# Optimization experiments

Hardware: AMD Instinct MI355X
Metric: run time of the kernel (lower is better)

Reference implementation:

```python
import jax, jax.numpy as jnp
import numpy as np

L = 2048      # max_length / encoder sequence length
E = 1024      # eo_hidden_size
H = 1024      # hidden_size
D = 512       # embed_size
V = 32000     # vocab_size
MV = 32768    # max_vocab_size


def setup_inputs() -> dict:
    key = jax.random.key(0)
    ks = jax.random.split(key, 20)
    s = 0.02
    return {
        "inp": jax.random.randint(ks[0], (1,), 0, V),
        "hidden": jax.random.normal(ks[1], (1, 1, H), jnp.float32),
        "encoder_outputs": jax.random.normal(ks[2], (L, E), jnp.float32),
        "input_seq": jax.random.randint(ks[3], (L,), 0, MV),
        "pre_prob": jax.random.randint(ks[4], (L,), 0, 2),
        "emb": jax.random.normal(ks[5], (V, D), jnp.float32) * s,
        "attn_W": jax.random.normal(ks[6], (L, H + D), jnp.float32) * s,
        "attn_b": jnp.zeros((L,), jnp.float32),
        "comb_W": jax.random.normal(ks[7], (H, E + D), jnp.float32) * s,
        "comb_b": jnp.zeros((H,), jnp.float32),
        "W_ih": jax.random.normal(ks[8], (3 * H, H + E), jnp.float32) * s,
        "W_hh": jax.random.normal(ks[9], (3 * H, H), jnp.float32) * s,
        "b_ih": jnp.zeros((3 * H,), jnp.float32),
        "b_hh": jnp.zeros((3 * H,), jnp.float32),
        "Wo_W": jax.random.normal(ks[10], (V, H), jnp.float32) * s,
        "Wo_b": jnp.zeros((V,), jnp.float32),
        "Wc_W": jax.random.normal(ks[11], (H, E), jnp.float32) * s,
        "Wc_b": jnp.zeros((H,), jnp.float32),
    }


def reference(inp, hidden, encoder_outputs, input_seq, pre_prob,
              emb, attn_W, attn_b, comb_W, comb_b,
              W_ih, W_hh, b_ih, b_hh, Wo_W, Wo_b, Wc_W, Wc_b):
    tok = inp[0]
    # --- copy-mechanism selective read (int path, matches torch .long() trunc) ---
    sel_w = (input_seq == tok).astype(jnp.int32) * pre_prob.astype(jnp.int32)  # [L]
    eo_int = jax.lax.stop_gradient(encoder_outputs).astype(jnp.int32)          # trunc toward 0
    sel_reading = (sel_w @ eo_int).astype(jnp.float32)                          # [E]
    # --- embedding (OOV -> UNK id 2); dropout is identity in eval ---
    embed_idx = jnp.where(tok >= V, 2, tok)
    embedded = emb[embed_idx]                                                   # [D]
    h = hidden[0, 0]                                                            # [H]
    # --- attention over encoder outputs ---
    attn_weights = jax.nn.softmax(attn_W @ jnp.concatenate([embedded, h]) + attn_b)  # [L]
    attn_applied = attn_weights @ encoder_outputs                               # [E]
    out = jax.nn.relu(comb_W @ jnp.concatenate([embedded, attn_applied]) + comb_b)   # [H]
    # --- single GRU step (torch gate order: r, z, n) ---
    x = jnp.concatenate([out, sel_reading])                                     # [H+E]
    gi = W_ih @ x + b_ih
    gh = W_hh @ h + b_hh
    r = jax.nn.sigmoid(gi[:H] + gh[:H])
    z = jax.nn.sigmoid(gi[H:2 * H] + gh[H:2 * H])
    n = jnp.tanh(gi[2 * H:] + r * gh[2 * H:])
    h_new = (1.0 - z) * n + z * h                                               # [H]
    # --- generate vs copy scores ---
    score_g = Wo_W @ h_new + Wo_b                                               # [V]
    score_c = jnp.tanh(encoder_outputs @ Wc_W.T + Wc_b) @ h_new                 # [L]
    score = jax.nn.softmax(jnp.concatenate([score_g, score_c]))                 # [V+L]
    prob_g, prob_c = score[:V], score[V:]
    # pad generate probs to MV and scatter-add copy probs (== mm with one-hot)
    out1 = jnp.zeros((MV,), score.dtype).at[:V].set(prob_g)
    out1 = out1.at[input_seq].add(prob_c)
    out1 = jnp.where(out1 == 0, 1e-9, out1)
    out1 = out1.at[2].set(1e-9)
    out1 = jnp.log(out1)
    return (out1[None, :], h_new[None, None, :], attn_weights[None, :], prob_c[None, :])
```

## Files before the change

### kernel.cpp

```cpp
#include <hip/hip_runtime.h>
#include <math.h>

#define LQ 2048
#define EQ 1024
#define HQ 1024
#define DQ 512
#define VQ 32000
#define MVQ 32768

#define OUT1_OFF 0
#define HNEW_OFF 32768
#define AW_OFF   33792
#define PC_OFF   35840

#define PSZ 2097152
#define KSPLIT 4

typedef __attribute__((ext_vector_type(8))) short short8_t;
typedef __attribute__((ext_vector_type(8))) unsigned short ushort8_t;
typedef __attribute__((ext_vector_type(4))) float floatx4;

__device__ inline float wred(float v) {
    v += __shfl_down(v, 32);
    v += __shfl_down(v, 16);
    v += __shfl_down(v, 8);
    v += __shfl_down(v, 4);
    v += __shfl_down(v, 2);
    v += __shfl_down(v, 1);
    return v;
}
__device__ inline float wred_max(float v) {
    v = fmaxf(v, __shfl_down(v, 32));
    v = fmaxf(v, __shfl_down(v, 16));
    v = fmaxf(v, __shfl_down(v, 8));
    v = fmaxf(v, __shfl_down(v, 4));
    v = fmaxf(v, __shfl_down(v, 2));
    v = fmaxf(v, __shfl_down(v, 1));
    return v;
}
__device__ inline float sigmoidf_(float x) { return 1.0f / (1.0f + expf(-x)); }
__device__ inline unsigned short f2bf(float x) {
    unsigned int u = __float_as_uint(x);
    unsigned int r = (u + 0x7fffu + ((u >> 16) & 1u)) >> 16;
    return (unsigned short)r;
}
__device__ inline float bf2f(unsigned short b) {
    return __uint_as_float(((unsigned int)b) << 16);
}
__device__ __forceinline__ void gload16(const unsigned short* g,
                                        unsigned short* l) {
    __builtin_amdgcn_global_load_lds(
        (const __attribute__((address_space(1))) unsigned int*)g,
        (__attribute__((address_space(3))) unsigned int*)l, 16, 0, 0);
}

__global__ __launch_bounds__(256) void k_prep(
    const float* __restrict__ enc, const float* __restrict__ Wc,
    const int* __restrict__ inp, const int* __restrict__ input_seq,
    const int* __restrict__ pre_prob,
    const float* __restrict__ attn_W, const float* __restrict__ attn_b,
    const float* __restrict__ emb, const float* __restrict__ hidden,
    unsigned short* __restrict__ Ah, unsigned short* __restrict__ Al,
    unsigned short* __restrict__ Bh, unsigned short* __restrict__ Bl,
    float* __restrict__ x2, float* __restrict__ logits, float* __restrict__ aa)
{
    __shared__ int s_cnt;
    __shared__ int s_list[LQ];
    const int tid = threadIdx.x;
    const int bx = blockIdx.x;
    if (bx < 512) {
        if (bx < 4) aa[bx * 256 + tid] = 0.0f;
        int warp = tid >> 6, lane = tid & 63;
        int r = bx * 4 + warp;
        int tok = inp[0];
        int ei = (tok >= VQ) ? 2 : tok;
        const float4* Wr = (const float4*)(attn_W + (size_t)r * 1536);
        const float4* e4 = (const float4*)(emb + (size_t)ei * DQ);
        const float4* h4 = (const float4*)hidden;
        float acc = 0.0f;
        #pragma unroll
        for (int i = 0; i < 6; ++i) {
            int idx = lane + i * 64;
            float4 x = (idx < 128) ? e4[idx] : h4[idx - 128];
            float4 w = Wr[idx];
            acc += w.x * x.x + w.y * x.y + w.z * x.z + w.w * x.w;
        }
        acc = wred(acc);
        if (lane == 0) logits[r] = acc + attn_b[r];
        return;
    }
    if (bx == 512) {
        if (tid == 0) s_cnt = 0;
        __syncthreads();
        int tok = inp[0];
        for (int l = tid; l < LQ; l += 256) {
            if (input_seq[l] == tok && pre_prob[l] != 0) {
                int p = atomicAdd(&s_cnt, 1);
                s_list[p] = l;
            }
        }
        __syncthreads();
        int nm = s_cnt;
        for (int e = tid; e < EQ; e += 256) {
            int acc = 0;
            for (int j = 0; j < nm; ++j)
                acc += (int)enc[(size_t)s_list[j] * EQ + e];
            x2[HQ + e] = (float)acc;
        }
        return;
    }
    size_t e0 = ((size_t)(bx - 513) * 256 + tid) * 8;
    const float* src;
    unsigned short *hdst, *ldst;
    size_t off;
    if (e0 < (size_t)LQ * EQ) { src = enc; hdst = Ah; ldst = Al; off = e0; }
    else { src = Wc; hdst = Bh; ldst = Bl; off = e0 - (size_t)LQ * EQ; }
    float4 v0 = *(const float4*)(src + off);
    float4 v1 = *(const float4*)(src + off + 4);
    float vv[8] = {v0.x, v0.y, v0.z, v0.w, v1.x, v1.y, v1.z, v1.w};
    ushort8_t H, L;
    #pragma unroll
    for (int k = 0; k < 8; ++k) {
        float x = vv[k];
        unsigned short hb = f2bf(x);
        H[k] = hb;
        L[k] = f2bf(x - bf2f(hb));
    }
    *(ushort8_t*)(hdst + off) = H;
    *(ushort8_t*)(ldst + off) = L;
}

__global__ __launch_bounds__(256, 2) void k_gemm_mfma(
    const unsigned short* __restrict__ Ah, const unsigned short* __restrict__ Al,
    const unsigned short* __restrict__ Bh, const unsigned short* __restrict__ Bl,
    float* __restrict__ P)
{
    __shared__ unsigned short sm[4 * 8192];
    const int t = threadIdx.x;
    const int lane = t & 63, wid = t >> 6;
    const int n0 = blockIdx.x * 128;
    const int m0 = blockIdx.y * 128;
    const int kz = blockIdx.z * 256;
    float* Pz = P + (size_t)blockIdx.z * PSZ;

    const unsigned short* tsrc =
        (wid == 0) ? Ah + (size_t)m0 * EQ :
        (wid == 1) ? Al + (size_t)m0 * EQ :
        (wid == 2) ? Bh + (size_t)n0 * EQ :
                     Bl + (size_t)n0 * EQ;
    unsigned short* tdst = sm + wid * 8192;

    const int srow = lane >> 3;
    const int schunk = lane & 7;
    const int wm = (wid >> 1) * 64, wn = (wid & 1) * 64;
    const int fr = lane & 15, kg = lane >> 4;

    floatx4 acc[4][4];
    #pragma unroll
    for (int i = 0; i < 4; ++i)
        #pragma unroll
        for (int j = 0; j < 4; ++j)
            acc[i][j] = (floatx4){0.f, 0.f, 0.f, 0.f};

    for (int s = 0; s < 4; ++s) {
        #pragma unroll
        for (int c = 0; c < 16; ++c) {
            int row = c * 8 + srow;
            int gch = schunk ^ (row & 7);
            gload16(tsrc + (size_t)row * EQ + kz + s * 64 + gch * 8,
                    tdst + c * 512);
        }
        __syncthreads();
        #pragma unroll
        for (int kk = 0; kk < 2; ++kk) {
            short8_t fah[4], fal[4], fbh[4], fbl[4];
            #pragma unroll
            for (int f = 0; f < 4; ++f) {
                int rowa = wm + f * 16 + fr;
                int ba = rowa * 128 + ((kk * 4 + kg) ^ (rowa & 7)) * 16;
                fah[f] = *(const short8_t*)((const char*)sm + ba);
                fal[f] = *(const short8_t*)((const char*)sm + 16384 + ba);
                int rowb = wn + f * 16 + fr;
                int bb = rowb * 128 + ((kk * 4 + kg) ^ (rowb & 7)) * 16;
                fbh[f] = *(const short8_t*)((const char*)sm + 32768 + bb);
                fbl[f] = *(const short8_t*)((const char*)sm + 49152 + bb);
            }
            #pragma unroll
            for (int i = 0; i < 4; ++i)
                #pragma unroll
                for (int j = 0; j < 4; ++j) {
                    acc[i][j] = __builtin_amdgcn_mfma_f32_16x16x32_bf16(
                        fah[i], fbh[j], acc[i][j], 0, 0, 0);
                    acc[i][j] = __builtin_amdgcn_mfma_f32_16x16x32_bf16(
                        fal[i], fbh[j], acc[i][j], 0, 0, 0);
                    acc[i][j] = __builtin_amdgcn_mfma_f32_16x16x32_bf16(
                        fah[i], fbl[j], acc[i][j], 0, 0, 0);
                }
        }
        __syncthreads();
    }
    #pragma unroll
    for (int i = 0; i < 4; ++i)
        #pragma unroll
        for (int j = 0; j < 4; ++j) {
            int row = m0 + wm + i * 16 + kg * 4;
            int col = n0 + wn + j * 16 + fr;
            #pragma unroll
            for (int r = 0; r < 4; ++r)
                Pz[(size_t)(row + r) * HQ + col] = acc[i][j][r];
        }
}

__global__ __launch_bounds__(256) void k_attn_sm_apply(
    const float* __restrict__ logits, const float* __restrict__ enc,
    float* __restrict__ aa, float* __restrict__ aw_out)
{
    __shared__ float sred[4];
    __shared__ float s_w[128];
    int tid = threadIdx.x, wid = tid >> 6, lane = tid & 63;
    float m = -3.4e38f;
    for (int i = tid; i < LQ; i += 256) m = fmaxf(m, logits[i]);
    m = wred_max(m);
    if (lane == 0) sred[wid] = m;
    __syncthreads();
    if (tid == 0)
        sred[0] = fmaxf(fmaxf(sred[0], sred[1]), fmaxf(sred[2], sred[3]));
    __syncthreads();
    m = sred[0];
    __syncthreads();
    float s = 0.0f;
    for (int i = tid; i < LQ; i += 256) s += expf(logits[i] - m);
    s = wred(s);
    if (lane == 0) sred[wid] = s;
    __syncthreads();
    if (tid == 0) sred[0] = sred[0] + sred[1] + sred[2] + sred[3];
    __syncthreads();
    s = sred[0];
    int l0 = blockIdx.y * 128;
    if (tid < 128) {
        float w = expf(logits[l0 + tid] - m) / s;
        s_w[tid] = w;
        if (blockIdx.x == 0) aw_out[l0 + tid] = w;
    }
    __syncthreads();
    int e = blockIdx.x * 256 + tid;
    float acc = 0.0f;
    for (int l = 0; l < 128; ++l)
        acc = fmaf(s_w[l], enc[(size_t)(l0 + l) * EQ + e], acc);
    atomicAdd(&aa[e], acc);
}

__global__ __launch_bounds__(256) void k_comb(
    const float* __restrict__ W, const float* __restrict__ b,
    const int* __restrict__ inp, const float* __restrict__ emb,
    const float* __restrict__ aa, float* __restrict__ x2)
{
    int warp = threadIdx.x >> 6, lane = threadIdx.x & 63;
    int r = blockIdx.x * 4 + warp;
    int tok = inp[0];
    int ei = (tok >= VQ) ? 2 : tok;
    const float4* Wr = (const float4*)(W + (size_t)r * 1536);
    const float4* e4 = (const float4*)(emb + (size_t)ei * DQ);
    const float4* a4 = (const float4*)aa;
    float acc = 0.0f;
    #pragma unroll
    for (int i = 0; i < 6; ++i) {
        int idx = lane + i * 64;
        float4 x = (idx < 128) ? e4[idx] : a4[idx - 128];
        float4 w = Wr[idx];
        acc += w.x * x.x + w.y * x.y + w.z * x.z + w.w * x.w;
    }
    acc = wred(acc);
    if (lane == 0) x2[r] = fmaxf(acc + b[r], 0.0f);
}

__global__ __launch_bounds__(256) void k_gru(
    const float* __restrict__ W_ih, const float* __restrict__ W_hh,
    const float* __restrict__ b_ih, const float* __restrict__ b_hh,
    const float* __restrict__ x2, const float* __restrict__ h,
    float* __restrict__ hnew, float* __restrict__ out_h)
{
    int warp = threadIdx.x >> 6, lane = threadIdx.x & 63;
    int i = blockIdx.x * 4 + warp;
    const float4* xv = (const float4*)x2;
    const float4* hv = (const float4*)h;
    const float4* Wr = (const float4*)(W_ih + (size_t)i * 2048);
    const float4* Wz = (const float4*)(W_ih + (size_t)(HQ + i) * 2048);
    const float4* Wn = (const float4*)(W_ih + (size_t)(2 * HQ + i) * 2048);
    const float4* Ur = (const float4*)(W_hh + (size_t)i * 1024);
    const float4* Uz = (const float4*)(W_hh + (size_t)(HQ + i) * 1024);
    const float4* Un = (const float4*)(W_hh + (size_t)(2 * HQ + i) * 1024);
    float ar = 0, az = 0, an = 0, br = 0, bz = 0, bn = 0;
    #pragma unroll
    for (int c = 0; c < 8; ++c) {
        int idx = lane + c * 64;
        float4 x = xv[idx];
        float4 w = Wr[idx]; ar += w.x*x.x + w.y*x.y + w.z*x.z + w.w*x.w;
        w = Wz[idx];        az += w.x*x.x + w.y*x.y + w.z*x.z + w.w*x.w;
        w = Wn[idx];        an += w.x*x.x + w.y*x.y + w.z*x.z + w.w*x.w;
    }
    #pragma unroll
    for (int c = 0; c < 4; ++c) {
        int idx = lane + c * 64;
        float4 x = hv[idx];
        float4 w = Ur[idx]; br += w.x*x.x + w.y*x.y + w.z*x.z + w.w*x.w;
        w = Uz[idx];        bz += w.x*x.x + w.y*x.y + w.z*x.z + w.w*x.w;
        w = Un[idx];        bn += w.x*x.x + w.y*x.y + w.z*x.z + w.w*x.w;
    }
    ar = wred(ar); az = wred(az); an = wred(an);
    br = wred(br); bz = wred(bz); bn = wred(bn);
    if (lane == 0) {
        float r = sigmoidf_(ar + b_ih[i] + br + b_hh[i]);
        float z = sigmoidf_(az + b_ih[HQ + i] + bz + b_hh[HQ + i]);
        float n = tanhf(an + b_ih[2 * HQ + i] + r * (bn + b_hh[2 * HQ + i]));
        float hn = (1.0f - z) * n + z * h[i];
        hnew[i] = hn;
        out_h[i] = hn;
    }
}

__global__ __launch_bounds__(256) void k_scores(
    const float* __restrict__ Wo_W, const float* __restrict__ Wo_b,
    const float* __restrict__ P, const float* __restrict__ Wc_b,
    const float* __restrict__ hnew, float* __restrict__ score)
{
    int warp = threadIdx.x >> 6, lane = threadIdx.x & 63;
    int r = blockIdx.x * 4 + warp;
    const float4* hv = (const float4*)hnew;
    float acc = 0.0f;
    if (r < VQ) {
        const float4* Wr = (const float4*)(Wo_W + (size_t)r * HQ);
        #pragma unroll
        for (int i = 0; i < 4; ++i) {
            int idx = lane + i * 64;
            float4 w = Wr[idx], x = hv[idx];
            acc += w.x * x.x + w.y * x.y + w.z * x.z + w.w * x.w;
        }
        acc = wred(acc);
        if (lane == 0) score[r] = acc + Wo_b[r];
    } else {
        int l = r - VQ;
        const float4* P0 = (const float4*)(P + (size_t)l * HQ);
        const float4* P1 = (const float4*)(P + (size_t)PSZ + (size_t)l * HQ);
        const float4* P2 = (const float4*)(P + 2 * (size_t)PSZ + (size_t)l * HQ);
        const float4* P3 = (const float4*)(P + 3 * (size_t)PSZ + (size_t)l * HQ);
        #pragma unroll
        for (int i = 0; i < 4; ++i) {
            int idx = lane + i * 64;
            float4 a = P0[idx], b1 = P1[idx], b2 = P2[idx], b3 = P3[idx];
            float4 bb = *(const float4*)(Wc_b + idx * 4);
            float4 x = hv[idx];
            acc += tanhf(a.x + b1.x + b2.x + b3.x + bb.x) * x.x +
                   tanhf(a.y + b1.y + b2.y + b3.y + bb.y) * x.y +
                   tanhf(a.z + b1.z + b2.z + b3.z + bb.z) * x.z +
                   tanhf(a.w + b1.w + b2.w + b3.w + bb.w) * x.w;
        }
        acc = wred(acc);
        if (lane == 0) score[VQ + l] = acc;
    }
}

__global__ __launch_bounds__(256) void k_final(
    const float* __restrict__ score, const int* __restrict__ input_seq,
    float* __restrict__ out1, float* __restrict__ out_pc)
{
    __shared__ float sred[4];
    __shared__ float bins[256];
    const int N = VQ + LQ;
    int tid = threadIdx.x, wid = tid >> 6, lane = tid & 63;
    float m = -3.4e38f;
    for (int i = tid; i < N; i += 256) m = fmaxf(m, score[i]);
    m = wred_max(m);
    if (lane == 0) sred[wid] = m;
    __syncthreads();
    if (tid == 0)
        sred[0] = fmaxf(fmaxf(sred[0], sred[1]), fmaxf(sred[2], sred[3]));
    __syncthreads();
    m = sred[0];
    __syncthreads();
    float s = 0.0f;
    for (int i = tid; i < N; i += 256) s += expf(score[i] - m);
    s = wred(s);
    if (lane == 0) sred[wid] = s;
    __syncthreads();
    if (tid == 0) sred[0] = sred[0] + sred[1] + sred[2] + sred[3];
    __syncthreads();
    s = sred[0];
    bins[tid] = 0.0f;
    __syncthreads();
    int i0 = blockIdx.x * 256;
    for (int l = tid; l < LQ; l += 256) {
        int si = input_seq[l];
        if (si >= i0 && si < i0 + 256)
            atomicAdd(&bins[si - i0], expf(score[VQ + l] - m) / s);
    }
    if (blockIdx.x < 8) {
        int l = blockIdx.x * 256 + tid;
        out_pc[l] = expf(score[VQ + l] - m) / s;
    }
    __syncthreads();
    int i = i0 + tid;
    float v = ((i < VQ) ? expf(score[i] - m) / s : 0.0f) + bins[tid];
    if (i == 2 || v == 0.0f) v = 1e-9f;
    out1[i] = logf(v);
}

extern "C" void kernel_launch(void* const* d_in, const int* in_sizes, int n_in,
                              void* d_out, int out_size, void* d_ws, size_t ws_size,
                              hipStream_t stream) {
    const int*   inp       = (const int*)  d_in[0];
    const float* hidden    = (const float*)d_in[1];
    const float* enc       = (const float*)d_in[2];
    const int*   input_seq = (const int*)  d_in[3];
    const int*   pre_prob  = (const int*)  d_in[4];
    const float* emb       = (const float*)d_in[5];
    const float* attn_W    = (const float*)d_in[6];
    const float* attn_b    = (const float*)d_in[7];
    const float* comb_W    = (const float*)d_in[8];
    const float* comb_b    = (const float*)d_in[9];
    const float* W_ih      = (const float*)d_in[10];
    const float* W_hh      = (const float*)d_in[11];
    const float* b_ih      = (const float*)d_in[12];
    const float* b_hh      = (const float*)d_in[13];
    const float* Wo_W      = (const float*)d_in[14];
    const float* Wo_b      = (const float*)d_in[15];
    const float* Wc_W      = (const float*)d_in[16];
    const float* Wc_b      = (const float*)d_in[17];

    float* out = (float*)d_out;

    unsigned short* Ah = (unsigned short*)d_ws;
    unsigned short* Al = Ah + (size_t)LQ * EQ;
    unsigned short* Bh = Al + (size_t)LQ * EQ;
    unsigned short* Bl = Bh + (size_t)HQ * EQ;
    float* P      = (float*)(Bl + (size_t)HQ * EQ);
    float* x2     = P + (size_t)KSPLIT * PSZ;
    float* hnew   = x2 + 2048;
    float* logits = hnew + 1024;
    float* aa     = logits + 2048;
    float* score  = aa + 1024;

    k_prep<<<2049, 256, 0, stream>>>(enc, Wc_W, inp, input_seq, pre_prob,
                                     attn_W, attn_b, emb, hidden,
                                     Ah, Al, Bh, Bl, x2, logits, aa);
    k_gemm_mfma<<<dim3(HQ / 128, LQ / 128, KSPLIT), 256, 0, stream>>>(
        Ah, Al, Bh, Bl, P);
    k_attn_sm_apply<<<dim3(EQ / 256, 16), 256, 0, stream>>>(logits, enc, aa,
                                                            out + AW_OFF);
    k_comb<<<HQ / 4, 256, 0, stream>>>(comb_W, comb_b, inp, emb, aa, x2);
    k_gru<<<HQ / 4, 256, 0, stream>>>(W_ih, W_hh, b_ih, b_hh, x2, hidden,
                                      hnew, out + HNEW_OFF);
    k_scores<<<(VQ + LQ) / 4, 256, 0, stream>>>(Wo_W, Wo_b, P, Wc_b, hnew,
                                                score);
    k_final<<<MVQ / 256, 256, 0, stream>>>(score, input_seq, out + OUT1_OFF,
                                           out + PC_OFF);
}
```

Measured before the change: 124.0 us.

## Fuse post-GEMM decoder stages into one cooperative kernel with grid syncs

Replaces the five small launches (attention softmax/apply, combine, GRU, scores, final softmax/scatter) and the non-conversion parts of the prep kernel with a single cooperative kernel of 512 blocks that uses grid-wide syncs between stages. The aim is to remove per-launch overhead and tail gaps between dependent small kernels. In exchange, the scores stage now loops over rows with fewer blocks, grid.sync costs replace launch boundaries, and the attention logits and selective read no longer overlap with the bf16 split conversion but run after the GEMM.

Result: slower. 395.4 us (+219.0%).

```diff
diff --git a/kernel.cpp b/kernel.cpp
--- a/kernel.cpp
+++ b/kernel.cpp
@@ -1,5 +1,8 @@
 #include <hip/hip_runtime.h>
+#include <hip/hip_cooperative_groups.h>
 #include <math.h>
+
+namespace cg = cooperative_groups;
 
 #define LQ 2048
 #define EQ 1024
@@ -54,62 +57,12 @@
         (__attribute__((address_space(3))) unsigned int*)l, 16, 0, 0);
 }
 
-__global__ __launch_bounds__(256) void k_prep(
+__global__ __launch_bounds__(256) void k_prep_split(
     const float* __restrict__ enc, const float* __restrict__ Wc,
-    const int* __restrict__ inp, const int* __restrict__ input_seq,
-    const int* __restrict__ pre_prob,
-    const float* __restrict__ attn_W, const float* __restrict__ attn_b,
-    const float* __restrict__ emb, const float* __restrict__ hidden,
     unsigned short* __restrict__ Ah, unsigned short* __restrict__ Al,
-    unsigned short* __restrict__ Bh, unsigned short* __restrict__ Bl,
-    float* __restrict__ x2, float* __restrict__ logits, float* __restrict__ aa)
+    unsigned short* __restrict__ Bh, unsigned short* __restrict__ Bl)
 {
-    __shared__ int s_cnt;
-    __shared__ int s_list[LQ];
-    const int tid = threadIdx.x;
-    const int bx = blockIdx.x;
-    if (bx < 512) {
-        if (bx < 4) aa[bx * 256 + tid] = 0.0f;
-        int warp = tid >> 6, lane = tid & 63;
-        int r = bx * 4 + warp;
-        int tok = inp[0];
-        int ei = (tok >= VQ) ? 2 : tok;
-        const float4* Wr = (const float4*)(attn_W + (size_t)r * 1536);
-        const float4* e4 = (const float4*)(emb + (size_t)ei * DQ);
-        const float4* h4 = (const float4*)hidden;
-        float acc = 0.0f;
-        #pragma unroll
-        for (int i = 0; i < 6; ++i) {
-            int idx = lane + i * 64;
-            float4 x = (idx < 128) ? e4[idx] : h4[idx - 128];
-            float4 w = Wr[idx];
-            acc += w.x * x.x + w.y * x.y + w.z * x.z + w.w * x.w;
-        }
-        acc = wred(acc);
-        if (lane == 0) logits[r] = acc + attn_b[r];
-        return;
-    }
-    if (bx == 512) {
-        if (tid == 0) s_cnt = 0;
-        __syncthreads();
-        int tok = inp[0];
-        for (int l = tid; l < LQ; l += 256) {
-            if (input_seq[l] == tok && pre_prob[l] != 0) {
-                int p = atomicAdd(&s_cnt, 1);
-                s_list[p] = l;
-            }
-        }
-        __syncthreads();
-        int nm = s_cnt;
-        for (int e = tid; e < EQ; e += 256) {
-            int acc = 0;
-            for (int j = 0; j < nm; ++j)
-                acc += (int)enc[(size_t)s_list[j] * EQ + e];
-            x2[HQ + e] = (float)acc;
-        }
-        return;
-    }
-    size_t e0 = ((size_t)(bx - 513) * 256 + tid) * 8;
+    size_t e0 = ((size_t)blockIdx.x * 256 + threadIdx.x) * 8;
     const float* src;
     unsigned short *hdst, *ldst;
     size_t off;
@@ -211,198 +164,245 @@
         }
 }
 
-__global__ __launch_bounds__(256) void k_attn_sm_apply(
-    const float* __restrict__ logits, const float* __restrict__ enc,
-    float* __restrict__ aa, float* __restrict__ aw_out)
+__global__ __launch_bounds__(256) void k_mega(
+    const float* __restrict__ enc, const int* __restrict__ inp,
+    const int* __restrict__ input_seq, const int* __restrict__ pre_prob,
+    const float* __restrict__ emb, const float* __restrict__ hidden,
+    const float* __restrict__ attn_W, const float* __restrict__ attn_b,
+    const float* __restrict__ comb_W, const float* __restrict__ comb_b,
+    const float* __restrict__ W_ih, const float* __restrict__ W_hh,
+    const float* __restrict__ b_ih, const float* __restrict__ b_hh,
+    const float* __restrict__ Wo_W, const float* __restrict__ Wo_b,
+    const float* __restrict__ Wc_b, const float* __restrict__ P,
+    float* __restrict__ x2, float* __restrict__ logits, float* __restrict__ aa,
+    float* __restrict__ hnew, float* __restrict__ score,
+    float* __restrict__ out1, float* __restrict__ out_pc,
+    float* __restrict__ out_aw, float* __restrict__ out_h)
 {
+    __shared__ int s_cnt;
+    __shared__ int s_list[LQ];
     __shared__ float sred[4];
     __shared__ float s_w[128];
-    int tid = threadIdx.x, wid = tid >> 6, lane = tid & 63;
-    float m = -3.4e38f;
-    for (int i = tid; i < LQ; i += 256) m = fmaxf(m, logits[i]);
-    m = wred_max(m);
-    if (lane == 0) sred[wid] = m;
-    __syncthreads();
-    if (tid == 0)
-        sred[0] = fmaxf(fmaxf(sred[0], sred[1]), fmaxf(sred[2], sred[3]));
-    __syncthreads();
-    m = sred[0];
-    __syncthreads();
-    float s = 0.0f;
-    for (int i = tid; i < LQ; i += 256) s += expf(logits[i] - m);
-    s = wred(s);
-    if (lane == 0) sred[wid] = s;
-    __syncthreads();
-    if (tid == 0) sred[0] = sred[0] + sred[1] + sred[2] + sred[3];
-    __syncthreads();
-    s = sred[0];
-    int l0 = blockIdx.y * 128;
-    if (tid < 128) {
-        float w = expf(logits[l0 + tid] - m) / s;
-        s_w[tid] = w;
-        if (blockIdx.x == 0) aw_out[l0 + tid] = w;
-    }
-    __syncthreads();
-    int e = blockIdx.x * 256 + tid;
-    float acc = 0.0f;
-    for (int l = 0; l < 128; ++l)
-        acc = fmaf(s_w[l], enc[(size_t)(l0 + l) * EQ + e], acc);
-    atomicAdd(&aa[e], acc);
-}
-
-__global__ __launch_bounds__(256) void k_comb(
-    const float* __restrict__ W, const float* __restrict__ b,
-    const int* __restrict__ inp, const float* __restrict__ emb,
-    const float* __restrict__ aa, float* __restrict__ x2)
-{
-    int warp = threadIdx.x >> 6, lane = threadIdx.x & 63;
-    int r = blockIdx.x * 4 + warp;
-    int tok = inp[0];
-    int ei = (tok >= VQ) ? 2 : tok;
-    const float4* Wr = (const float4*)(W + (size_t)r * 1536);
-    const float4* e4 = (const float4*)(emb + (size_t)ei * DQ);
-    const float4* a4 = (const float4*)aa;
-    float acc = 0.0f;
-    #pragma unroll
-    for (int i = 0; i < 6; ++i) {
-        int idx = lane + i * 64;
-        float4 x = (idx < 128) ? e4[idx] : a4[idx - 128];
-        float4 w = Wr[idx];
-        acc += w.x * x.x + w.y * x.y + w.z * x.z + w.w * x.w;
-    }
-    acc = wred(acc);
-    if (lane == 0) x2[r] = fmaxf(acc + b[r], 0.0f);
-}
-
-__global__ __launch_bounds__(256) void k_gru(
-    const float* __restrict__ W_ih, const float* __restrict__ W_hh,
-    const float* __restrict__ b_ih, const float* __restrict__ b_hh,
-    const float* __restrict__ x2, const float* __restrict__ h,
-    float* __restrict__ hnew, float* __restrict__ out_h)
-{
-    int warp = threadIdx.x >> 6, lane = threadIdx.x & 63;
-    int i = blockIdx.x * 4 + warp;
-    const float4* xv = (const float4*)x2;
-    const float4* hv = (const float4*)h;
-    const float4* Wr = (const float4*)(W_ih + (size_t)i * 2048);
-    const float4* Wz = (const float4*)(W_ih + (size_t)(HQ + i) * 2048);
-    const float4* Wn = (const float4*)(W_ih + (size_t)(2 * HQ + i) * 2048);
-    const float4* Ur = (const float4*)(W_hh + (size_t)i * 1024);
-    const float4* Uz = (const float4*)(W_hh + (size_t)(HQ + i) * 1024);
-    const float4* Un = (const float4*)(W_hh + (size_t)(2 * HQ + i) * 1024);
-    float ar = 0, az = 0, an = 0, br = 0, bz = 0, bn = 0;
-    #pragma unroll
-    for (int c = 0; c < 8; ++c) {
-        int idx = lane + c * 64;
-        float4 x = xv[idx];
-        float4 w = Wr[idx]; ar += w.x*x.x + w.y*x.y + w.z*x.z + w.w*x.w;
-        w = Wz[idx];        az += w.x*x.x + w.y*x.y + w.z*x.z + w.w*x.w;
-        w = Wn[idx];        an += w.x*x.x + w.y*x.y + w.z*x.z + w.w*x.w;
-    }
-    #pragma unroll
-    for (int c = 0; c < 4; ++c) {
-        int idx = lane + c * 64;
-        float4 x = hv[idx];
-        float4 w = Ur[idx]; br += w.x*x.x + w.y*x.y + w.z*x.z + w.w*x.w;
-        w = Uz[idx];        bz += w.x*x.x + w.y*x.y + w.z*x.z + w.w*x.w;
-        w = Un[idx];        bn += w.x*x.x + w.y*x.y + w.z*x.z + w.w*x.w;
-    }
-    ar = wred(ar); az = wred(az); an = wred(an);
-    br = wred(br); bz = wred(bz); bn = wred(bn);
-    if (lane == 0) {
-        float r = sigmoidf_(ar + b_ih[i] + br + b_hh[i]);
-        float z = sigmoidf_(az + b_ih[HQ + i] + bz + b_hh[HQ + i]);
-        float n = tanhf(an + b_ih[2 * HQ + i] + r * (bn + b_hh[2 * HQ + i]));
-        float hn = (1.0f - z) * n + z * h[i];
-        hnew[i] = hn;
-        out_h[i] = hn;
-    }
-}
-
-__global__ __launch_bounds__(256) void k_scores(
-    const float* __restrict__ Wo_W, const float* __restrict__ Wo_b,
-    const float* __restrict__ P, const float* __restrict__ Wc_b,
-    const float* __restrict__ hnew, float* __restrict__ score)
-{
-    int warp = threadIdx.x >> 6, lane = threadIdx.x & 63;
-    int r = blockIdx.x * 4 + warp;
-    const float4* hv = (const float4*)hnew;
-    float acc = 0.0f;
-    if (r < VQ) {
-        const float4* Wr = (const float4*)(Wo_W + (size_t)r * HQ);
+    __shared__ float bins[256];
+
+    cg::grid_group grid = cg::this_grid();
+    const int bx = blockIdx.x, tid = threadIdx.x;
+    const int warp = tid >> 6, lane = tid & 63;
+    const int tok = inp[0];
+    const int ei = (tok >= VQ) ? 2 : tok;
+
+    {
+        if (bx < 4) aa[bx * 256 + tid] = 0.0f;
+        int r = bx * 4 + warp;
+        const float4* Wr = (const float4*)(attn_W + (size_t)r * 1536);
+        const float4* e4 = (const float4*)(emb + (size_t)ei * DQ);
+        const float4* h4 = (const float4*)hidden;
+        float acc = 0.0f;
         #pragma unroll
-        for (int i = 0; i < 4; ++i) {
+        for (int i = 0; i < 6; ++i) {
             int idx = lane + i * 64;
-            float4 w = Wr[idx], x = hv[idx];
+            float4 x = (idx < 128) ? e4[idx] : h4[idx - 128];
+            float4 w = Wr[idx];
             acc += w.x * x.x + w.y * x.y + w.z * x.z + w.w * x.w;
         }
         acc = wred(acc);
-        if (lane == 0) score[r] = acc + Wo_b[r];
-    } else {
-        int l = r - VQ;
-        const float4* P0 = (const float4*)(P + (size_t)l * HQ);
-        const float4* P1 = (const float4*)(P + (size_t)PSZ + (size_t)l * HQ);
-        const float4* P2 = (const float4*)(P + 2 * (size_t)PSZ + (size_t)l * HQ);
-        const float4* P3 = (const float4*)(P + 3 * (size_t)PSZ + (size_t)l * HQ);
-        #pragma unroll
-        for (int i = 0; i < 4; ++i) {
-            int idx = lane + i * 64;
-            float4 a = P0[idx], b1 = P1[idx], b2 = P2[idx], b3 = P3[idx];
-            float4 bb = *(const float4*)(Wc_b + idx * 4);
-            float4 x = hv[idx];
-            acc += tanhf(a.x + b1.x + b2.x + b3.x + bb.x) * x.x +
-                   tanhf(a.y + b1.y + b2.y + b3.y + bb.y) * x.y +
-                   tanhf(a.z + b1.z + b2.z + b3.z + bb.z) * x.z +
-                   tanhf(a.w + b1.w + b2.w + b3.w + bb.w) * x.w;
-        }
-        acc = wred(acc);
-        if (lane == 0) score[VQ + l] = acc;
-    }
-}
-
-__global__ __launch_bounds__(256) void k_final(
-    const float* __restrict__ score, const int* __restrict__ input_seq,
-    float* __restrict__ out1, float* __restrict__ out_pc)
-{
-    __shared__ float sred[4];
-    __shared__ float bins[256];
-    const int N = VQ + LQ;
-    int tid = threadIdx.x, wid = tid >> 6, lane = tid & 63;
-    float m = -3.4e38f;
-    for (int i = tid; i < N; i += 256) m = fmaxf(m, score[i]);
-    m = wred_max(m);
-    if (lane == 0) sred[wid] = m;
-    __syncthreads();
-    if (tid == 0)
-        sred[0] = fmaxf(fmaxf(sred[0], sred[1]), fmaxf(sred[2], sred[3]));
-    __syncthreads();
-    m = sred[0];
-    __syncthreads();
-    float s = 0.0f;
-    for (int i = tid; i < N; i += 256) s += expf(score[i] - m);
-    s = wred(s);
-    if (lane == 0) sred[wid] = s;
-    __syncthreads();
-    if (tid == 0) sred[0] = sred[0] + sred[1] + sred[2] + sred[3];
-    __syncthreads();
-    s = sred[0];
-    bins[tid] = 0.0f;
-    __syncthreads();
-    int i0 = blockIdx.x * 256;
-    for (int l = tid; l < LQ; l += 256) {
-        int si = input_seq[l];
-        if (si >= i0 && si < i0 + 256)
-            atomicAdd(&bins[si - i0], expf(score[VQ + l] - m) / s);
-    }
-    if (blockIdx.x < 8) {
-        int l = blockIdx.x * 256 + tid;
-        out_pc[l] = expf(score[VQ + l] - m) / s;
-    }
-    __syncthreads();
-    int i = i0 + tid;
-    float v = ((i < VQ) ? expf(score[i] - m) / s : 0.0f) + bins[tid];
-    if (i == 2 || v == 0.0f) v = 1e-9f;
-    out1[i] = logf(v);
+        if (lane == 0) logits[r] = acc + attn_b[r];
+    }
+    if (bx == 4) {
+        if (tid == 0) s_cnt = 0;
+        __syncthreads();
+        for (int l = tid; l < LQ; l += 256) {
+            if (input_seq[l] == tok && pre_prob[l] != 0) {
+                int p = atomicAdd(&s_cnt, 1);
+                s_list[p] = l;
+            }
+        }
+        __syncthreads();
+        int nm = s_cnt;
+        for (int e = tid; e < EQ; e += 256) {
+            int acc = 0;
+            for (int j = 0; j < nm; ++j)
+                acc += (int)enc[(size_t)s_list[j] * EQ + e];
+            x2[HQ + e] = (float)acc;
+        }
+    }
+    grid.sync();
+
+    if (bx < 64) {
+        int xb = bx & 3, yb = bx >> 2;
+        float m = -3.4e38f;
+        for (int i = tid; i < LQ; i += 256) m = fmaxf(m, logits[i]);
+        m = wred_max(m);
+        if (lane == 0) sred[warp] = m;
+        __syncthreads();
+        if (tid == 0)
+            sred[0] = fmaxf(fmaxf(sred[0], sred[1]), fmaxf(sred[2], sred[3]));
+        __syncthreads();
+        m = sred[0];
+        __syncthreads();
+        float s = 0.0f;
+        for (int i = tid; i < LQ; i += 256) s += expf(logits[i] - m);
+        s = wred(s);
+        if (lane == 0) sred[warp] = s;
+        __syncthreads();
+        if (tid == 0) sred[0] = sred[0] + sred[1] + sred[2] + sred[3];
+        __syncthreads();
+        s = sred[0];
+        int l0 = yb * 128;
+        if (tid < 128) {
+            float w = expf(logits[l0 + tid] - m) / s;
+            s_w[tid] = w;
+            if (xb == 0) out_aw[l0 + tid] = w;
+        }
+        __syncthreads();
+        int e = xb * 256 + tid;
+        float acc = 0.0f;
+        for (int l = 0; l < 128; ++l)
+            acc = fmaf(s_w[l], enc[(size_t)(l0 + l) * EQ + e], acc);
+        atomicAdd(&aa[e], acc);
+    }
+    grid.sync();
+
+    {
+        int r = bx * 4 + warp;
+        if (r < HQ) {
+            const float4* Wr = (const float4*)(comb_W + (size_t)r * 1536);
+            const float4* e4 = (const float4*)(emb + (size_t)ei * DQ);
+            const float4* a4 = (const float4*)aa;
+            float acc = 0.0f;
+            #pragma unroll
+            for (int i = 0; i < 6; ++i) {
+                int idx = lane + i * 64;
+                float4 x = (idx < 128) ? e4[idx] : a4[idx - 128];
+                float4 w = Wr[idx];
+                acc += w.x * x.x + w.y * x.y + w.z * x.z + w.w * x.w;
+            }
+            acc = wred(acc);
+            if (lane == 0) x2[r] = fmaxf(acc + comb_b[r], 0.0f);
+        }
+    }
+    grid.sync();
+
+    {
+        int i = bx * 4 + warp;
+        if (i < HQ) {
+            const float4* xv = (const float4*)x2;
+            const float4* hv = (const float4*)hidden;
+            const float4* Wr = (const float4*)(W_ih + (size_t)i * 2048);
+            const float4* Wz = (const float4*)(W_ih + (size_t)(HQ + i) * 2048);
+            const float4* Wn = (const float4*)(W_ih + (size_t)(2 * HQ + i) * 2048);
+            const float4* Ur = (const float4*)(W_hh + (size_t)i * 1024);
+            const float4* Uz = (const float4*)(W_hh + (size_t)(HQ + i) * 1024);
+            const float4* Un = (const float4*)(W_hh + (size_t)(2 * HQ + i) * 1024);
+            float ar = 0, az = 0, an = 0, br = 0, bz = 0, bn = 0;
+            #pragma unroll
+            for (int c = 0; c < 8; ++c) {
+                int idx = lane + c * 64;
+                float4 x = xv[idx];
+                float4 w = Wr[idx]; ar += w.x*x.x + w.y*x.y + w.z*x.z + w.w*x.w;
+                w = Wz[idx];        az += w.x*x.x + w.y*x.y + w.z*x.z + w.w*x.w;
+                w = Wn[idx];        an += w.x*x.x + w.y*x.y + w.z*x.z + w.w*x.w;
+            }
+            #pragma unroll
+            for (int c = 0; c < 4; ++c) {
+                int idx = lane + c * 64;
+                float4 x = hv[idx];
+                float4 w = Ur[idx]; br += w.x*x.x + w.y*x.y + w.z*x.z + w.w*x.w;
+                w = Uz[idx];        bz += w.x*x.x + w.y*x.y + w.z*x.z + w.w*x.w;
+                w = Un[idx];        bn += w.x*x.x + w.y*x.y + w.z*x.z + w.w*x.w;
+            }
+            ar = wred(ar); az = wred(az); an = wred(an);
+            br = wred(br); bz = wred(bz); bn = wred(bn);
+            if (lane == 0) {
+                float r = sigmoidf_(ar + b_ih[i] + br + b_hh[i]);
+                float z = sigmoidf_(az + b_ih[HQ + i] + bz + b_hh[HQ + i]);
+                float n = tanhf(an + b_ih[2 * HQ + i] +
+                                r * (bn + b_hh[2 * HQ + i]));
+                float hn = (1.0f - z) * n + z * hidden[i];
+                hnew[i] = hn;
+                out_h[i] = hn;
+            }
+        }
+    }
+    grid.sync();
+
+    {
+        const float4* hv = (const float4*)hnew;
+        int w = bx * 4 + warp;
+        for (int r = w; r < VQ + LQ; r += 2048) {
+            float acc = 0.0f;
+            if (r < VQ) {
+                const float4* Wr = (const float4*)(Wo_W + (size_t)r * HQ);
+                #pragma unroll
+                for (int i = 0; i < 4; ++i) {
+                    int idx = lane + i * 64;
+                    float4 ww = Wr[idx], x = hv[idx];
+                    acc += ww.x * x.x + ww.y * x.y + ww.z * x.z + ww.w * x.w;
+                }
+                acc = wred(acc);
+                if (lane == 0) score[r] = acc + Wo_b[r];
+            } else {
+                int l = r - VQ;
+                const float4* P0 = (const float4*)(P + (size_t)l * HQ);
+                const float4* P1 = (const float4*)(P + (size_t)PSZ + (size_t)l * HQ);
+                const float4* P2 = (const float4*)(P + 2 * (size_t)PSZ + (size_t)l * HQ);
+                const float4* P3 = (const float4*)(P + 3 * (size_t)PSZ + (size_t)l * HQ);
+                #pragma unroll
+                for (int i = 0; i < 4; ++i) {
+                    int idx = lane + i * 64;
+                    float4 a = P0[idx], b1 = P1[idx], b2 = P2[idx], b3 = P3[idx];
+                    float4 bb = *(const float4*)(Wc_b + idx * 4);
+                    float4 x = hv[idx];
+                    acc += tanhf(a.x + b1.x + b2.x + b3.x + bb.x) * x.x +
+                           tanhf(a.y + b1.y + b2.y + b3.y + bb.y) * x.y +
+                           tanhf(a.z + b1.z + b2.z + b3.z + bb.z) * x.z +
+                           tanhf(a.w + b1.w + b2.w + b3.w + bb.w) * x.w;
+                }
+                acc = wred(acc);
+                if (lane == 0) score[r] = acc;
+            }
+        }
+    }
+    grid.sync();
+
+    if (bx < 128) {
+        const int N = VQ + LQ;
+        float m = -3.4e38f;
+        for (int i = tid; i < N; i += 256) m = fmaxf(m, score[i]);
+        m = wred_max(m);
+        if (lane == 0) sred[warp] = m;
+        __syncthreads();
+        if (tid == 0)
+            sred[0] = fmaxf(fmaxf(sred[0], sred[1]), fmaxf(sred[2], sred[3]));
+        __syncthreads();
+        m = sred[0];
+        __syncthreads();
+        float s = 0.0f;
+        for (int i = tid; i < N; i += 256) s += expf(score[i] - m);
+        s = wred(s);
+        if (lane == 0) sred[warp] = s;
+        __syncthreads();
+        if (tid == 0) sred[0] = sred[0] + sred[1] + sred[2] + sred[3];
+        __syncthreads();
+        s = sred[0];
+        bins[tid] = 0.0f;
+        __syncthreads();
+        int i0 = bx * 256;
+        for (int l = tid; l < LQ; l += 256) {
+            int si = input_seq[l];
+            if (si >= i0 && si < i0 + 256)
+                atomicAdd(&bins[si - i0], expf(score[VQ + l] - m) / s);
+        }
+        if (bx < 8) {
+            int l = bx * 256 + tid;
+            out_pc[l] = expf(score[VQ + l] - m) / s;
+        }
+        __syncthreads();
+        int i = i0 + tid;
+        float v = ((i < VQ) ? expf(score[i] - m) / s : 0.0f) + bins[tid];
+        if (i == 2 || v == 0.0f) v = 1e-9f;
+        out1[i] = logf(v);
+    }
 }
 
 extern "C" void kernel_launch(void* const* d_in, const int* in_sizes, int n_in,
@@ -440,18 +440,22 @@
     float* aa     = logits + 2048;
     float* score  = aa + 1024;
 
-    k_prep<<<2049, 256, 0, stream>>>(enc, Wc_W, inp, input_seq, pre_prob,
-                                     attn_W, attn_b, emb, hidden,
-                                     Ah, Al, Bh, Bl, x2, logits, aa);
+    k_prep_split<<<1536, 256, 0, stream>>>(enc, Wc_W, Ah, Al, Bh, Bl);
     k_gemm_mfma<<<dim3(HQ / 128, LQ / 128, KSPLIT), 256, 0, stream>>>(
         Ah, Al, Bh, Bl, P);
-    k_attn_sm_apply<<<dim3(EQ / 256, 16), 256, 0, stream>>>(logits, enc, aa,
-                                                            out + AW_OFF);
-    k_comb<<<HQ / 4, 256, 0, stream>>>(comb_W, comb_b, inp, emb, aa, x2);
-    k_gru<<<HQ / 4, 256, 0, stream>>>(W_ih, W_hh, b_ih, b_hh, x2, hidden,
-                                      hnew, out + HNEW_OFF);
-    k_scores<<<(VQ + LQ) / 4, 256, 0, stream>>>(Wo_W, Wo_b, P, Wc_b, hnew,
-                                                score);
-    k_final<<<MVQ / 256, 256, 0, stream>>>(score, input_seq, out + OUT1_OFF,
-                                           out + PC_OFF);
-}
+
+    float* out1   = out + OUT1_OFF;
+    float* out_pc = out + PC_OFF;
+    float* out_aw = out + AW_OFF;
+    float* out_h  = out + HNEW_OFF;
+    void* margs[] = {
+        (void*)&enc, (void*)&inp, (void*)&input_seq, (void*)&pre_prob,
+        (void*)&emb, (void*)&hidden, (void*)&attn_W, (void*)&attn_b,
+        (void*)&comb_W, (void*)&comb_b, (void*)&W_ih, (void*)&W_hh,
+        (void*)&b_ih, (void*)&b_hh, (void*)&Wo_W, (void*)&Wo_b,
+        (void*)&Wc_b, (void*)&P, (void*)&x2, (void*)&logits, (void*)&aa,
+        (void*)&hnew, (void*)&score, (void*)&out1, (void*)&out_pc,
+        (void*)&out_aw, (void*)&out_h};
+    hipLaunchCooperativeKernel((const void*)k_mega, dim3(512), dim3(256),
+                               margs, 0, stream);
+}
```

## Fuse attention apply and independent GEMV partials into double-buffered MFMA GEMM launch

Applied to the files above, without the earlier changes.

Merges the split-K MFMA GEMM, the attention softmax/apply, and the input-independent GEMV parts (W_ih selective-read half, W_hh·h, comb_W·embedding) into one heterogeneous launch. Different block ranges do different jobs so the bandwidth-bound GEMVs overlap with the compute-bound GEMM. The GEMM switches to a double-buffered K=32 stage with a new LDS swizzle, halving shared memory per stage. The later comb and GRU kernels read less weight data because the precomputed partials are passed in. The cost is extra global scratch buffers and more complex block dispatch, which may unbalance work across CUs.

Result: faster. 120.5 us (-2.8%).

```diff
diff --git a/kernel.cpp b/kernel.cpp
--- a/kernel.cpp
+++ b/kernel.cpp
@@ -130,60 +130,74 @@
     *(ushort8_t*)(ldst + off) = L;
 }
 
-__global__ __launch_bounds__(256, 2) void k_gemm_mfma(
+__global__ __launch_bounds__(256, 2) void k_gemm_fused(
     const unsigned short* __restrict__ Ah, const unsigned short* __restrict__ Al,
     const unsigned short* __restrict__ Bh, const unsigned short* __restrict__ Bl,
-    float* __restrict__ P)
+    float* __restrict__ P,
+    const float* __restrict__ logits, const float* __restrict__ enc,
+    float* __restrict__ aa, float* __restrict__ aw_out,
+    const float* __restrict__ W_ih, const float* __restrict__ W_hh,
+    const float* __restrict__ comb_W, const int* __restrict__ inp,
+    const float* __restrict__ emb, const float* __restrict__ hidden,
+    const float* __restrict__ x2,
+    float* __restrict__ gi_sel, float* __restrict__ gh_pre,
+    float* __restrict__ pre_c)
 {
-    __shared__ unsigned short sm[4 * 8192];
-    const int t = threadIdx.x;
+    __shared__ unsigned short sm[2 * 4 * 4096];
+    const int b = blockIdx.x, t = threadIdx.x;
     const int lane = t & 63, wid = t >> 6;
-    const int n0 = blockIdx.x * 128;
-    const int m0 = blockIdx.y * 128;
-    const int kz = blockIdx.z * 256;
-    float* Pz = P + (size_t)blockIdx.z * PSZ;
-
-    const unsigned short* tsrc =
-        (wid == 0) ? Ah + (size_t)m0 * EQ :
-        (wid == 1) ? Al + (size_t)m0 * EQ :
-        (wid == 2) ? Bh + (size_t)n0 * EQ :
-                     Bl + (size_t)n0 * EQ;
-    unsigned short* tdst = sm + wid * 8192;
-
-    const int srow = lane >> 3;
-    const int schunk = lane & 7;
-    const int wm = (wid >> 1) * 64, wn = (wid & 1) * 64;
-    const int fr = lane & 15, kg = lane >> 4;
-
-    floatx4 acc[4][4];
-    #pragma unroll
-    for (int i = 0; i < 4; ++i)
-        #pragma unroll
-        for (int j = 0; j < 4; ++j)
-            acc[i][j] = (floatx4){0.f, 0.f, 0.f, 0.f};
-
-    for (int s = 0; s < 4; ++s) {
-        #pragma unroll
-        for (int c = 0; c < 16; ++c) {
-            int row = c * 8 + srow;
-            int gch = schunk ^ (row & 7);
-            gload16(tsrc + (size_t)row * EQ + kz + s * 64 + gch * 8,
-                    tdst + c * 512);
-        }
-        __syncthreads();
-        #pragma unroll
-        for (int kk = 0; kk < 2; ++kk) {
+
+    if (b < 512) {
+        const int n0 = (b & 7) * 128;
+        const int m0 = ((b >> 3) & 15) * 128;
+        const int zz = b >> 7;
+        const int kz = zz * 256;
+        float* Pz = P + (size_t)zz * PSZ;
+        const unsigned short* tsrc =
+            (wid == 0) ? Ah + (size_t)m0 * EQ :
+            (wid == 1) ? Al + (size_t)m0 * EQ :
+            (wid == 2) ? Bh + (size_t)n0 * EQ :
+                         Bl + (size_t)n0 * EQ;
+        const int srow = lane >> 2, schunk = lane & 3;
+        const int wm = (wid >> 1) * 64, wn = (wid & 1) * 64;
+        const int fr = lane & 15, kg = lane >> 4;
+
+        floatx4 acc[4][4];
+        #pragma unroll
+        for (int i = 0; i < 4; ++i)
+            #pragma unroll
+            for (int j = 0; j < 4; ++j)
+                acc[i][j] = (floatx4){0.f, 0.f, 0.f, 0.f};
+
+        #define STAGE(buf, s)                                                  \
+            {                                                                  \
+                unsigned short* dst = sm + (buf) * 16384 + wid * 4096;         \
+                _Pragma("unroll")                                              \
+                for (int c = 0; c < 8; ++c) {                                  \
+                    int row = c * 16 + srow;                                   \
+                    int gch = schunk ^ ((row >> 1) & 3);                       \
+                    gload16(tsrc + (size_t)row * EQ + kz + (s) * 32 + gch * 8, \
+                            dst + c * 512);                                    \
+                }                                                              \
+            }
+
+        STAGE(0, 0);
+        __syncthreads();
+        for (int s = 0; s < 8; ++s) {
+            int cur = s & 1;
+            if (s < 7) STAGE(cur ^ 1, s + 1);
+            const char* base = (const char*)sm + cur * 32768;
             short8_t fah[4], fal[4], fbh[4], fbl[4];
             #pragma unroll
             for (int f = 0; f < 4; ++f) {
-                int rowa = wm + f * 16 + fr;
-                int ba = rowa * 128 + ((kk * 4 + kg) ^ (rowa & 7)) * 16;
-                fah[f] = *(const short8_t*)((const char*)sm + ba);
-                fal[f] = *(const short8_t*)((const char*)sm + 16384 + ba);
-                int rowb = wn + f * 16 + fr;
-                int bb = rowb * 128 + ((kk * 4 + kg) ^ (rowb & 7)) * 16;
-                fbh[f] = *(const short8_t*)((const char*)sm + 32768 + bb);
-                fbl[f] = *(const short8_t*)((const char*)sm + 49152 + bb);
+                int ra = wm + f * 16 + fr;
+                int oa = ra * 64 + ((kg ^ ((ra >> 1) & 3)) * 16);
+                fah[f] = *(const short8_t*)(base + oa);
+                fal[f] = *(const short8_t*)(base + 8192 + oa);
+                int rb = wn + f * 16 + fr;
+                int ob = rb * 64 + ((kg ^ ((rb >> 1) & 3)) * 16);
+                fbh[f] = *(const short8_t*)(base + 16384 + ob);
+                fbl[f] = *(const short8_t*)(base + 24576 + ob);
             }
             #pragma unroll
             for (int i = 0; i < 4; ++i)
@@ -196,86 +210,129 @@
                     acc[i][j] = __builtin_amdgcn_mfma_f32_16x16x32_bf16(
                         fah[i], fbl[j], acc[i][j], 0, 0, 0);
                 }
-        }
-        __syncthreads();
-    }
-    #pragma unroll
-    for (int i = 0; i < 4; ++i)
-        #pragma unroll
-        for (int j = 0; j < 4; ++j) {
-            int row = m0 + wm + i * 16 + kg * 4;
-            int col = n0 + wn + j * 16 + fr;
+            __syncthreads();
+        }
+        #pragma unroll
+        for (int i = 0; i < 4; ++i)
             #pragma unroll
-            for (int r = 0; r < 4; ++r)
-                Pz[(size_t)(row + r) * HQ + col] = acc[i][j][r];
-        }
-}
-
-__global__ __launch_bounds__(256) void k_attn_sm_apply(
-    const float* __restrict__ logits, const float* __restrict__ enc,
-    float* __restrict__ aa, float* __restrict__ aw_out)
-{
-    __shared__ float sred[4];
-    __shared__ float s_w[128];
-    int tid = threadIdx.x, wid = tid >> 6, lane = tid & 63;
-    float m = -3.4e38f;
-    for (int i = tid; i < LQ; i += 256) m = fmaxf(m, logits[i]);
-    m = wred_max(m);
-    if (lane == 0) sred[wid] = m;
-    __syncthreads();
-    if (tid == 0)
-        sred[0] = fmaxf(fmaxf(sred[0], sred[1]), fmaxf(sred[2], sred[3]));
-    __syncthreads();
-    m = sred[0];
-    __syncthreads();
-    float s = 0.0f;
-    for (int i = tid; i < LQ; i += 256) s += expf(logits[i] - m);
-    s = wred(s);
-    if (lane == 0) sred[wid] = s;
-    __syncthreads();
-    if (tid == 0) sred[0] = sred[0] + sred[1] + sred[2] + sred[3];
-    __syncthreads();
-    s = sred[0];
-    int l0 = blockIdx.y * 128;
-    if (tid < 128) {
-        float w = expf(logits[l0 + tid] - m) / s;
-        s_w[tid] = w;
-        if (blockIdx.x == 0) aw_out[l0 + tid] = w;
-    }
-    __syncthreads();
-    int e = blockIdx.x * 256 + tid;
-    float acc = 0.0f;
-    for (int l = 0; l < 128; ++l)
-        acc = fmaf(s_w[l], enc[(size_t)(l0 + l) * EQ + e], acc);
-    atomicAdd(&aa[e], acc);
+            for (int j = 0; j < 4; ++j) {
+                int row = m0 + wm + i * 16 + kg * 4;
+                int col = n0 + wn + j * 16 + fr;
+                #pragma unroll
+                for (int r = 0; r < 4; ++r)
+                    Pz[(size_t)(row + r) * HQ + col] = acc[i][j][r];
+            }
+        return;
+    }
+    if (b < 576) {
+        float* sred = (float*)sm;
+        float* s_w  = (float*)sm + 8;
+        int sb = b - 512;
+        int xb = sb & 3, yb = sb >> 2;
+        float m = -3.4e38f;
+        for (int i = t; i < LQ; i += 256) m = fmaxf(m, logits[i]);
+        m = wred_max(m);
+        if (lane == 0) sred[wid] = m;
+        __syncthreads();
+        if (t == 0)
+            sred[0] = fmaxf(fmaxf(sred[0], sred[1]), fmaxf(sred[2], sred[3]));
+        __syncthreads();
+        m = sred[0];
+        __syncthreads();
+        float s = 0.0f;
+        for (int i = t; i < LQ; i += 256) s += expf(logits[i] - m);
+        s = wred(s);
+        if (lane == 0) sred[wid] = s;
+        __syncthreads();
+        if (t == 0) sred[0] = sred[0] + sred[1] + sred[2] + sred[3];
+        __syncthreads();
+        s = sred[0];
+        int l0 = yb * 128;
+        if (t < 128) {
+            float w = expf(logits[l0 + t] - m) / s;
+            s_w[t] = w;
+            if (xb == 0) aw_out[l0 + t] = w;
+        }
+        __syncthreads();
+        int e = xb * 256 + t;
+        float acc = 0.0f;
+        for (int l = 0; l < 128; ++l)
+            acc = fmaf(s_w[l], enc[(size_t)(l0 + l) * EQ + e], acc);
+        atomicAdd(&aa[e], acc);
+        return;
+    }
+    if (b < 1344) {
+        int row = (b - 576) * 4 + wid;
+        const float4* Wr = (const float4*)(W_ih + (size_t)row * 2048 + 1024);
+        const float4* xs = (const float4*)(x2 + HQ);
+        float acc = 0.0f;
+        #pragma unroll
+        for (int c = 0; c < 4; ++c) {
+            int idx = lane + c * 64;
+            float4 w = Wr[idx], x = xs[idx];
+            acc += w.x * x.x + w.y * x.y + w.z * x.z + w.w * x.w;
+        }
+        acc = wred(acc);
+        if (lane == 0) gi_sel[row] = acc;
+        return;
+    }
+    if (b < 2112) {
+        int row = (b - 1344) * 4 + wid;
+        const float4* Wr = (const float4*)(W_hh + (size_t)row * 1024);
+        const float4* hv = (const float4*)hidden;
+        float acc = 0.0f;
+        #pragma unroll
+        for (int c = 0; c < 4; ++c) {
+            int idx = lane + c * 64;
+            float4 w = Wr[idx], x = hv[idx];
+            acc += w.x * x.x + w.y * x.y + w.z * x.z + w.w * x.w;
+        }
+        acc = wred(acc);
+        if (lane == 0) gh_pre[row] = acc;
+        return;
+    }
+    {
+        int row = (b - 2112) * 4 + wid;
+        int tok = inp[0];
+        int ei = (tok >= VQ) ? 2 : tok;
+        const float4* Wr = (const float4*)(comb_W + (size_t)row * 1536);
+        const float4* e4 = (const float4*)(emb + (size_t)ei * DQ);
+        float acc = 0.0f;
+        #pragma unroll
+        for (int c = 0; c < 2; ++c) {
+            int idx = lane + c * 64;
+            float4 w = Wr[idx], x = e4[idx];
+            acc += w.x * x.x + w.y * x.y + w.z * x.z + w.w * x.w;
+        }
+        acc = wred(acc);
+        if (lane == 0) pre_c[row] = acc;
+        return;
+    }
 }
 
 __global__ __launch_bounds__(256) void k_comb(
     const float* __restrict__ W, const float* __restrict__ b,
-    const int* __restrict__ inp, const float* __restrict__ emb,
-    const float* __restrict__ aa, float* __restrict__ x2)
+    const float* __restrict__ pre_c, const float* __restrict__ aa,
+    float* __restrict__ x2)
 {
     int warp = threadIdx.x >> 6, lane = threadIdx.x & 63;
     int r = blockIdx.x * 4 + warp;
-    int tok = inp[0];
-    int ei = (tok >= VQ) ? 2 : tok;
-    const float4* Wr = (const float4*)(W + (size_t)r * 1536);
-    const float4* e4 = (const float4*)(emb + (size_t)ei * DQ);
+    const float4* Wr = (const float4*)(W + (size_t)r * 1536 + 512);
     const float4* a4 = (const float4*)aa;
     float acc = 0.0f;
     #pragma unroll
-    for (int i = 0; i < 6; ++i) {
+    for (int i = 0; i < 4; ++i) {
         int idx = lane + i * 64;
-        float4 x = (idx < 128) ? e4[idx] : a4[idx - 128];
-        float4 w = Wr[idx];
+        float4 w = Wr[idx], x = a4[idx];
         acc += w.x * x.x + w.y * x.y + w.z * x.z + w.w * x.w;
     }
     acc = wred(acc);
-    if (lane == 0) x2[r] = fmaxf(acc + b[r], 0.0f);
+    if (lane == 0) x2[r] = fmaxf(acc + pre_c[r] + b[r], 0.0f);
 }
 
 __global__ __launch_bounds__(256) void k_gru(
-    const float* __restrict__ W_ih, const float* __restrict__ W_hh,
+    const float* __restrict__ W_ih, const float* __restrict__ gi_sel,
+    const float* __restrict__ gh_pre,
     const float* __restrict__ b_ih, const float* __restrict__ b_hh,
     const float* __restrict__ x2, const float* __restrict__ h,
     float* __restrict__ hnew, float* __restrict__ out_h)
@@ -283,36 +340,29 @@
     int warp = threadIdx.x >> 6, lane = threadIdx.x & 63;
     int i = blockIdx.x * 4 + warp;
     const float4* xv = (const float4*)x2;
-    const float4* hv = (const float4*)h;
     const float4* Wr = (const float4*)(W_ih + (size_t)i * 2048);
     const float4* Wz = (const float4*)(W_ih + (size_t)(HQ + i) * 2048);
     const float4* Wn = (const float4*)(W_ih + (size_t)(2 * HQ + i) * 2048);
-    const float4* Ur = (const float4*)(W_hh + (size_t)i * 1024);
-    const float4* Uz = (const float4*)(W_hh + (size_t)(HQ + i) * 1024);
-    const float4* Un = (const float4*)(W_hh + (size_t)(2 * HQ + i) * 1024);
-    float ar = 0, az = 0, an = 0, br = 0, bz = 0, bn = 0;
+    float ar = 0, az = 0, an = 0;
     #pragma unroll
-    for (int c = 0; c < 8; ++c) {
+    for (int c = 0; c < 4; ++c) {
         int idx = lane + c * 64;
         float4 x = xv[idx];
         float4 w = Wr[idx]; ar += w.x*x.x + w.y*x.y + w.z*x.z + w.w*x.w;
         w = Wz[idx];        az += w.x*x.x + w.y*x.y + w.z*x.z + w.w*x.w;
         w = Wn[idx];        an += w.x*x.x + w.y*x.y + w.z*x.z + w.w*x.w;
     }
-    #pragma unroll
-    for (int c = 0; c < 4; ++c) {
-        int idx = lane + c * 64;
-        float4 x = hv[idx];
-        float4 w = Ur[idx]; br += w.x*x.x + w.y*x.y + w.z*x.z + w.w*x.w;
-        w = Uz[idx];        bz += w.x*x.x + w.y*x.y + w.z*x.z + w.w*x.w;
-        w = Un[idx];        bn += w.x*x.x + w.y*x.y + w.z*x.z + w.w*x.w;
-    }
     ar = wred(ar); az = wred(az); an = wred(an);
-    br = wred(br); bz = wred(bz); bn = wred(bn);
     if (lane == 0) {
-        float r = sigmoidf_(ar + b_ih[i] + br + b_hh[i]);
-        float z = sigmoidf_(az + b_ih[HQ + i] + bz + b_hh[HQ + i]);
-        float n = tanhf(an + b_ih[2 * HQ + i] + r * (bn + b_hh[2 * HQ + i]));
+        float gir = ar + gi_sel[i] + b_ih[i];
+        float giz = az + gi_sel[HQ + i] + b_ih[HQ + i];
+        float gin = an + gi_sel[2 * HQ + i] + b_ih[2 * HQ + i];
+        float ghr = gh_pre[i] + b_hh[i];
+        float ghz = gh_pre[HQ + i] + b_hh[HQ + i];
+        float ghn = gh_pre[2 * HQ + i] + b_hh[2 * HQ + i];
+        float r = sigmoidf_(gir + ghr);
+        float z = sigmoidf_(giz + ghz);
+        float n = tanhf(gin + r * ghn);
         float hn = (1.0f - z) * n + z * h[i];
         hnew[i] = hn;
         out_h[i] = hn;
@@ -439,17 +489,20 @@
     float* logits = hnew + 1024;
     float* aa     = logits + 2048;
     float* score  = aa + 1024;
+    float* gi_sel = score + 34048;
+    float* gh_pre = gi_sel + 3072;
+    float* pre_c  = gh_pre + 3072;
 
     k_prep<<<2049, 256, 0, stream>>>(enc, Wc_W, inp, input_seq, pre_prob,
                                      attn_W, attn_b, emb, hidden,
                                      Ah, Al, Bh, Bl, x2, logits, aa);
-    k_gemm_mfma<<<dim3(HQ / 128, LQ / 128, KSPLIT), 256, 0, stream>>>(
-        Ah, Al, Bh, Bl, P);
-    k_attn_sm_apply<<<dim3(EQ / 256, 16), 256, 0, stream>>>(logits, enc, aa,
-                                                            out + AW_OFF);
-    k_comb<<<HQ / 4, 256, 0, stream>>>(comb_W, comb_b, inp, emb, aa, x2);
-    k_gru<<<HQ / 4, 256, 0, stream>>>(W_ih, W_hh, b_ih, b_hh, x2, hidden,
-                                      hnew, out + HNEW_OFF);
+    k_gemm_fused<<<2368, 256, 0, stream>>>(Ah, Al, Bh, Bl, P, logits, enc,
+                                           aa, out + AW_OFF, W_ih, W_hh,
+                                           comb_W, inp, emb, hidden, x2,
+                                           gi_sel, gh_pre, pre_c);
+    k_comb<<<HQ / 4, 256, 0, stream>>>(comb_W, comb_b, pre_c, aa, x2);
+    k_gru<<<HQ / 4, 256, 0, stream>>>(W_ih, gi_sel, gh_pre, b_ih, b_hh, x2,
+                                      hidden, hnew, out + HNEW_OFF);
     k_scores<<<(VQ + LQ) / 4, 256, 0, stream>>>(Wo_W, Wo_b, P, Wc_b, hnew,
                                                 score);
     k_final<<<MVQ / 256, 256, 0, stream>>>(score, input_seq, out + OUT1_OFF,
```
